# Kernel optimization log

Measured on AMD Instinct MI355X. Metric: run time of the kernel, lower is better.

Reference implementation:

```python
import jax, jax.numpy as jnp
import numpy as np

D_MODEL = 1024
NHEAD = 16
D_K = D_MODEL // NHEAD
NEG_INF = -1e30


def setup_inputs() -> dict:
    key = jax.random.key(0)
    ks = jax.random.split(key, 5)
    seq, batch = 2048, 4
    scale_in = 1.0 / np.sqrt(D_MODEL)
    return {
        "x": jax.random.normal(ks[0], (seq, batch, D_MODEL), dtype=jnp.float32),
        # torch nn.Linear stores weight as (out_features, in_features)
        "w_qkv": jax.random.normal(ks[1], (3 * D_MODEL, D_MODEL), dtype=jnp.float32) * scale_in,
        "b_qkv": jax.random.normal(ks[2], (3 * D_MODEL,), dtype=jnp.float32) * 0.01,
        "w_out": jax.random.normal(ks[3], (D_MODEL, D_MODEL), dtype=jnp.float32) * scale_in,
        "b_out": jax.random.normal(ks[4], (D_MODEL,), dtype=jnp.float32) * 0.01,
        "causal": 1,
    }


def reference(x, w_qkv, b_qkv, w_out, b_out, causal):
    seq, batch, d_model = x.shape
    # fused QKV projection: (seq, batch, 3*d_model)
    qkv = jnp.einsum("sbd,ed->sbe", x, w_qkv) + b_qkv
    q, k, v = jnp.split(qkv, 3, axis=-1)

    def to_heads(t):
        # (seq, batch, d_model) -> (batch*nhead, seq, d_k)
        return t.reshape(seq, batch * NHEAD, D_K).transpose(1, 0, 2)

    q, k, v = to_heads(q), to_heads(k), to_heads(v)
    # full O(seq^2) score tensor, matching the manual implementation
    scores = jnp.einsum("hqd,hkd->hqk", q, k) / (D_K ** 0.5)
    if causal:  # causal is a static Python int, safe under jit as constant
        mask = jnp.triu(jnp.ones((seq, seq), dtype=bool), k=1)
        scores = jnp.where(mask[None, :, :], NEG_INF, scores)
    attn = jax.nn.softmax(scores, axis=-1)
    out = jnp.einsum("hqk,hkd->hqd", attn, v)  # (batch*nhead, seq, d_k)
    out = out.transpose(1, 0, 2).reshape(seq, batch, d_model)
    return jnp.einsum("sbd,ed->sbe", out, w_out) + b_out
```

## Files before the change

### kernel.cpp

```cpp
#include <hip/hip_runtime.h>

typedef __attribute__((ext_vector_type(8))) short short8;
typedef __attribute__((ext_vector_type(4))) float floatx4;
typedef __attribute__((ext_vector_type(4))) unsigned short ushort4v;

__device__ __forceinline__ unsigned short f2bf(float f) {
  unsigned int u = __float_as_uint(f);
  u += 0x7FFFu + ((u >> 16) & 1u);
  return (unsigned short)(u >> 16);
}

__device__ __forceinline__ unsigned int cvt_pk_bf16(float lo, float hi) {
  unsigned int r;
  asm("v_cvt_pk_bf16_f32 %0, %1, %2" : "=v"(r) : "v"(lo), "v"(hi));
  return r;
}

__device__ __forceinline__ void async_copy16(const void* g, void* l) {
  __builtin_amdgcn_global_load_lds(
      (const __attribute__((address_space(1))) unsigned int*)g,
      (__attribute__((address_space(3))) unsigned int*)l, 16, 0, 0);
}

__device__ __forceinline__ float fexp2(float x) {
#if __has_builtin(__builtin_amdgcn_exp2f)
  return __builtin_amdgcn_exp2f(x);
#else
  return exp2f(x);
#endif
}

__global__ __launch_bounds__(256) void cvt_all(const float* __restrict__ x,
                                               const float* __restrict__ wq,
                                               const float* __restrict__ wo,
                                               unsigned short* __restrict__ Xb,
                                               unsigned short* __restrict__ Wqb,
                                               unsigned short* __restrict__ Wob) {
  int i = blockIdx.x * blockDim.x + threadIdx.x;
  const float* src;
  unsigned short* dst;
  int off;
  if (i < 2097152) { src = x;  dst = Xb;  off = i; }
  else if (i < 2883584) { src = wq; dst = Wqb; off = i - 2097152; }
  else { src = wo; dst = Wob; off = i - 2883584; }
  float4 v = reinterpret_cast<const float4*>(src)[off];
  ushort4v o;
  o[0] = f2bf(v.x); o[1] = f2bf(v.y); o[2] = f2bf(v.z); o[3] = f2bf(v.w);
  reinterpret_cast<ushort4v*>(dst)[off] = o;
}

template <int MODE, int NX>
__global__ __launch_bounds__(256, 4) void gemm_nt(const unsigned short* __restrict__ A,
                                                  const unsigned short* __restrict__ B,
                                                  const float* __restrict__ bias,
                                                  void* __restrict__ C,
                                                  int M, int N, int K) {
  __shared__ __align__(16) unsigned short lds[2][128 * 64];
  unsigned short* lA = lds[0];
  unsigned short* lB = lds[1];
  unsigned short* lflat = &lds[0][0];
  const int tid = threadIdx.x;
  const int lane = tid & 63, wave = tid >> 6;
  const int lr = lane & 15, lh = lane >> 4;
  const int chunk = gridDim.x >> 3;
  const int g2 = (blockIdx.x & 7) * chunk + (blockIdx.x >> 3);
  const int m0 = (g2 / NX) * 128, n0 = (g2 % NX) * 128;
  const int wm = (wave >> 1) * 64, wn = (wave & 1) * 64;
  floatx4 acc[4][4] = {};

  for (int k0 = 0; k0 < K; k0 += 64) {
    __syncthreads();
#pragma unroll
    for (int c0 = 0; c0 < 1024; c0 += 256) {
      int L = c0 + tid;
      int r = L >> 3;
      int c = (L & 7) ^ (r & 7);
      async_copy16(A + (size_t)(m0 + r) * K + k0 + c * 8, &lA[(size_t)(c0 + wave * 64) * 8]);
      async_copy16(B + (size_t)(n0 + r) * K + k0 + c * 8, &lB[(size_t)(c0 + wave * 64) * 8]);
    }
    __syncthreads();
#pragma unroll
    for (int kk = 0; kk < 2; ++kk) {
      short8 af[4], bfr[4];
#pragma unroll
      for (int mf = 0; mf < 4; ++mf)
        af[mf] = *(const short8*)&lA[(wm + mf * 16 + lr) * 64 + (((kk * 4 + lh) ^ (lr & 7)) * 8)];
#pragma unroll
      for (int nf = 0; nf < 4; ++nf)
        bfr[nf] = *(const short8*)&lB[(wn + nf * 16 + lr) * 64 + (((kk * 4 + lh) ^ (lr & 7)) * 8)];
#pragma unroll
      for (int mf = 0; mf < 4; ++mf)
#pragma unroll
        for (int nf = 0; nf < 4; ++nf)
          acc[mf][nf] = __builtin_amdgcn_mfma_f32_16x16x32_bf16(af[mf], bfr[nf], acc[mf][nf], 0, 0, 0);
    }
  }

  if (MODE == 1 && (n0 >> 10) == 2) {
    __syncthreads();
#pragma unroll
    for (int mf = 0; mf < 4; ++mf) {
      int sl = (wm >> 2) + mf * 4 + lh;
#pragma unroll
      for (int nf = 0; nf < 4; ++nf) {
        int cl = wn + nf * 16 + lr;
        int hh = cl >> 6, dd = cl & 63;
        int sx = sl ^ ((dd & 3) << 3);
#pragma unroll
        for (int r = 0; r < 4; ++r) {
          float v = acc[mf][nf][r] + bias[n0 + cl];
          lflat[((r * 2 + hh) * 64 + dd) * 32 + sx] = f2bf(v);
        }
      }
    }
    __syncthreads();
    const int hbase = (n0 & 1023) >> 6;
    const int s0g = m0 >> 2;
    unsigned short* V = (unsigned short*)C + (size_t)2 * 64 * 2048 * 64;
#pragma unroll
    for (int k = 0; k < 8; ++k) {
      int f = tid + k * 256;
      int p = f >> 2, q = f & 3;
      int b = p >> 7, hh = (p >> 6) & 1, dd = p & 63;
      int g = b * 16 + hbase + hh;
      int sc = (q ^ (dd & 3)) * 8;
      short8 vv = *(const short8*)&lflat[p * 32 + q * 8];
      *(short8*)&V[((size_t)g * 64 + dd) * 2048 + s0g + sc] = vv;
    }
  } else {
#pragma unroll
    for (int mf = 0; mf < 4; ++mf)
#pragma unroll
      for (int nf = 0; nf < 4; ++nf)
#pragma unroll
        for (int r = 0; r < 4; ++r) {
          int row = m0 + wm + mf * 16 + lh * 4 + r;
          int col = n0 + wn + nf * 16 + lr;
          float v = acc[mf][nf][r] + bias[col];
          if (MODE == 0) {
            ((float*)C)[(size_t)row * N + col] = v;
          } else {
            int part = col >> 10, wi = col & 1023;
            int h = wi >> 6, dd = wi & 63;
            int s = row >> 2, b = row & 3;
            int gg = b * 16 + h;
            size_t base = (size_t)part * (64u * 2048u * 64u);
            if (part == 0) v *= 0.18033688011112042f;
            ((unsigned short*)C)[base + ((size_t)gg * 2048 + s) * 64 + dd] = f2bf(v);
          }
        }
  }
}

__global__ __launch_bounds__(256, 3) void attn_fwd(const unsigned short* __restrict__ Qb,
                                                   const unsigned short* __restrict__ Kb,
                                                   const unsigned short* __restrict__ Vt,
                                                   unsigned short* __restrict__ Att,
                                                   const int* __restrict__ causal_p) {
  __shared__ __align__(16) unsigned short lK[2][64 * 64];
  __shared__ __align__(16) unsigned short lV[2][64 * 64];
  __shared__ __align__(16) unsigned short lP[4][32 * 64];
  const int tid = threadIdx.x;
  const int lane = tid & 63, w = tid >> 6;
  const int lr = lane & 15, lh = lane >> 4;
  const int bid = blockIdx.x;
  const int g = (bid & 7) + 8 * (bid >> 7);
  int qt = (bid >> 3) & 15;
  qt = (qt & 12) | ((qt ^ (qt >> 2)) & 3);
  const int q0 = qt * 128;
  const int causal = causal_p[0];
  const size_t headOff = (size_t)g * 2048 * 64;
  const size_t vtHead = (size_t)g * 64 * 2048;
  const int q0w = q0 + w * 32;

  short8 qf[2][2];
#pragma unroll
  for (int qb = 0; qb < 2; ++qb)
#pragma unroll
    for (int kf = 0; kf < 2; ++kf)
      qf[qb][kf] = *(const short8*)&Qb[headOff + (size_t)(q0w + qb * 16 + lr) * 64 + kf * 32 + lh * 8];

  floatx4 oacc[2][4] = {};
  float mrow[2] = {-1e30f, -1e30f}, lrow[2] = {0.f, 0.f};

  const int nt = causal ? (q0 + 128) / 64 : 2048 / 64;
  const int qmax_w = q0w + 31;

  auto stageK = [&](int buf, int kv0) {
#pragma unroll
    for (int c0 = 0; c0 < 512; c0 += 256) {
      int L = c0 + tid;
      int kvr = L >> 3;
      int c = (tid & 7) ^ (kvr & 7);
      async_copy16(Kb + headOff + (size_t)(kv0 + kvr) * 64 + c * 8,
                   &lK[buf][(size_t)(c0 + w * 64) * 8]);
    }
  };
  auto stageV = [&](int buf, int kv0) {
#pragma unroll
    for (int c0 = 0; c0 < 512; c0 += 256) {
      int L = c0 + tid;
      int dr = L >> 3;
      int c = (tid & 7) ^ (dr & 7);
      async_copy16(Vt + vtHead + (size_t)dr * 2048 + kv0 + c * 8,
                   &lV[buf][(size_t)(c0 + w * 64) * 8]);
    }
  };

  stageK(0, 0);
  stageV(0, 0);
  int cur = 0;

  for (int t = 0; t < nt; ++t) {
    const int kv0 = t * 64;
    if (t + 1 < nt) {
      stageK(cur ^ 1, kv0 + 64);
      stageV(cur ^ 1, kv0 + 64);
      asm volatile("s_waitcnt vmcnt(4)" ::: "memory");
    } else {
      asm volatile("s_waitcnt vmcnt(0)" ::: "memory");
    }
    __builtin_amdgcn_s_barrier();
    asm volatile("" ::: "memory");

    if (!causal || kv0 <= qmax_w) {
      floatx4 sacc[2][4] = {};
      __builtin_amdgcn_s_setprio(1);
#pragma unroll
      for (int kk = 0; kk < 2; ++kk) {
        short8 kfr[4];
#pragma unroll
        for (int nf = 0; nf < 4; ++nf)
          kfr[nf] = *(const short8*)&lK[cur][(nf * 16 + lr) * 64 + (((kk * 4 + lh) ^ (lr & 7)) * 8)];
#pragma unroll
        for (int qb = 0; qb < 2; ++qb)
#pragma unroll
          for (int nf = 0; nf < 4; ++nf)
            sacc[qb][nf] = __builtin_amdgcn_mfma_f32_16x16x32_bf16(kfr[nf], qf[qb][kk], sacc[qb][nf], 0, 0, 0);
      }
      __builtin_amdgcn_s_setprio(0);

      if (causal && kv0 + 63 > q0w) {
#pragma unroll
        for (int qb = 0; qb < 2; ++qb) {
          int q = q0w + qb * 16 + lr;
#pragma unroll
          for (int nf = 0; nf < 4; ++nf)
#pragma unroll
            for (int r = 0; r < 4; ++r) {
              int kv = kv0 + nf * 16 + lh * 4 + r;
              if (kv > q) sacc[qb][nf][r] = -1e30f;
            }
        }
      }

      float alpha[2];
#pragma unroll
      for (int qb = 0; qb < 2; ++qb) {
        float rm = -1e30f;
#pragma unroll
        for (int nf = 0; nf < 4; ++nf)
          rm = fmaxf(rm, fmaxf(fmaxf(sacc[qb][nf][0], sacc[qb][nf][1]),
                               fmaxf(sacc[qb][nf][2], sacc[qb][nf][3])));
        rm = fmaxf(rm, __shfl_xor(rm, 16, 64));
        rm = fmaxf(rm, __shfl_xor(rm, 32, 64));
        float mn = fmaxf(mrow[qb], rm);
        alpha[qb] = fexp2(mrow[qb] - mn);
        mrow[qb] = mn;
        float rs = 0.f;
#pragma unroll
        for (int nf = 0; nf < 4; ++nf)
#pragma unroll
          for (int r = 0; r < 4; ++r) {
            float p = fexp2(sacc[qb][nf][r] - mn);
            sacc[qb][nf][r] = p;
            rs += p;
          }
        rs += __shfl_xor(rs, 16, 64);
        rs += __shfl_xor(rs, 32, 64);
        lrow[qb] = lrow[qb] * alpha[qb] + rs;
      }

#pragma unroll
      for (int qb = 0; qb < 2; ++qb)
#pragma unroll
        for (int nf = 0; nf < 4; ++nf) {
          uint2 pk;
          pk.x = cvt_pk_bf16(sacc[qb][nf][0], sacc[qb][nf][1]);
          pk.y = cvt_pk_bf16(sacc[qb][nf][2], sacc[qb][nf][3]);
          int c = (2 * nf + (lh >> 1)) ^ (lr & 7);
          *(uint2*)&lP[w][(qb * 16 + lr) * 64 + c * 8 + (lh & 1) * 4] = pk;
        }

#pragma unroll
      for (int qb = 0; qb < 2; ++qb) {
        float at[4];
#pragma unroll
        for (int r = 0; r < 4; ++r)
          at[r] = __shfl(alpha[qb], lh * 4 + r, 64);
#pragma unroll
        for (int nd = 0; nd < 4; ++nd)
#pragma unroll
          for (int r = 0; r < 4; ++r)
            oacc[qb][nd][r] *= at[r];
      }

      __builtin_amdgcn_s_setprio(1);
#pragma unroll
      for (int kk = 0; kk < 2; ++kk) {
        short8 pf[2], vf[4];
#pragma unroll
        for (int qb = 0; qb < 2; ++qb)
          pf[qb] = *(const short8*)&lP[w][(qb * 16 + lr) * 64 + (((kk * 4 + lh) ^ (lr & 7)) * 8)];
#pragma unroll
        for (int nd = 0; nd < 4; ++nd)
          vf[nd] = *(const short8*)&lV[cur][(nd * 16 + lr) * 64 + (((kk * 4 + lh) ^ (lr & 7)) * 8)];
#pragma unroll
        for (int qb = 0; qb < 2; ++qb)
#pragma unroll
          for (int nd = 0; nd < 4; ++nd)
            oacc[qb][nd] = __builtin_amdgcn_mfma_f32_16x16x32_bf16(pf[qb], vf[nd], oacc[qb][nd], 0, 0, 0);
      }
      __builtin_amdgcn_s_setprio(0);
    }
    asm volatile("" ::: "memory");
    __builtin_amdgcn_s_barrier();
    cur ^= 1;
  }

  const int bb = g >> 4, hh = g & 15;
#pragma unroll
  for (int qb = 0; qb < 2; ++qb) {
    float invl = 1.f / lrow[qb];
    float it[4];
#pragma unroll
    for (int r = 0; r < 4; ++r)
      it[r] = __shfl(invl, lh * 4 + r, 64);
#pragma unroll
    for (int r = 0; r < 4; ++r) {
      int s = q0w + qb * 16 + lh * 4 + r;
#pragma unroll
      for (int nd = 0; nd < 4; ++nd) {
        int dd = nd * 16 + lr;
        Att[((size_t)s * 4 + bb) * 1024 + hh * 64 + dd] = f2bf(oacc[qb][nd][r] * it[r]);
      }
    }
  }
}

extern "C" void kernel_launch(void* const* d_in, const int* in_sizes, int n_in,
                              void* d_out, int out_size, void* d_ws, size_t ws_size,
                              hipStream_t stream) {
  const float* x     = (const float*)d_in[0];
  const float* w_qkv = (const float*)d_in[1];
  const float* b_qkv = (const float*)d_in[2];
  const float* w_out = (const float*)d_in[3];
  const float* b_out = (const float*)d_in[4];
  const int*   causal = (const int*)d_in[5];
  float* out = (float*)d_out;

  char* ws = (char*)d_ws;
  size_t off = 0;
  auto alloc = [&](size_t bytes) { char* p = ws + off; off += (bytes + 255) & ~(size_t)255; return p; };
  unsigned short* Xbf  = (unsigned short*)alloc((size_t)8192 * 1024 * 2);
  unsigned short* Wqkv = (unsigned short*)alloc((size_t)3072 * 1024 * 2);
  unsigned short* Wout = (unsigned short*)alloc((size_t)1024 * 1024 * 2);
  unsigned short* QKV  = (unsigned short*)alloc((size_t)3 * 64 * 2048 * 64 * 2);
  unsigned short* Att  = (unsigned short*)alloc((size_t)8192 * 1024 * 2);
  (void)ws_size; (void)in_sizes; (void)n_in; (void)out_size;

  cvt_all<<<12288, 256, 0, stream>>>(x, w_qkv, w_out, Xbf, Wqkv, Wout);

  gemm_nt<1, 24><<<24 * 64, 256, 0, stream>>>(Xbf, Wqkv, b_qkv, (void*)QKV, 8192, 3072, 1024);

  const unsigned short* Qh = QKV;
  const unsigned short* Kh = QKV + (size_t)64 * 2048 * 64;
  const unsigned short* Vh = QKV + (size_t)2 * 64 * 2048 * 64;
  attn_fwd<<<1024, 256, 0, stream>>>(Qh, Kh, Vh, Att, causal);

  gemm_nt<0, 8><<<8 * 64, 256, 0, stream>>>(Att, Wout, b_out, (void*)out, 8192, 1024, 1024);
}
```

Baseline: 176.2 us.

## Switch attention to 32x32x16 MFMA with register-resident P and staged output

Rewrites the attention inner loop to use 32x32x16 bf16 MFMA tiles, so each lane owns one query row. Row max and sum then need only one cross-lane shuffle, and the alpha broadcast shuffles go away. P is moved into the B-operand layout with lane-swap shuffles instead of a round trip through LDS, which removes the per-wave P buffer. The output is staged through shared memory so the global stores are 16-byte rows instead of scattered 2-byte writes. The launch-bounds occupancy hint is dropped, so register pressure and occupancy may change.

After: 176.7 us. About the same (+0.3%).

```diff
diff --git a/kernel.cpp b/kernel.cpp
--- a/kernel.cpp
+++ b/kernel.cpp
@@ -2,6 +2,7 @@
 
 typedef __attribute__((ext_vector_type(8))) short short8;
 typedef __attribute__((ext_vector_type(4))) float floatx4;
+typedef __attribute__((ext_vector_type(16))) float floatx16;
 typedef __attribute__((ext_vector_type(4))) unsigned short ushort4v;
 
 __device__ __forceinline__ unsigned short f2bf(float f) {
@@ -152,17 +153,15 @@
   }
 }
 
-__global__ __launch_bounds__(256, 3) void attn_fwd(const unsigned short* __restrict__ Qb,
-                                                   const unsigned short* __restrict__ Kb,
-                                                   const unsigned short* __restrict__ Vt,
-                                                   unsigned short* __restrict__ Att,
-                                                   const int* __restrict__ causal_p) {
-  __shared__ __align__(16) unsigned short lK[2][64 * 64];
-  __shared__ __align__(16) unsigned short lV[2][64 * 64];
-  __shared__ __align__(16) unsigned short lP[4][32 * 64];
+__global__ __launch_bounds__(256) void attn_fwd(const unsigned short* __restrict__ Qb,
+                                                const unsigned short* __restrict__ Kb,
+                                                const unsigned short* __restrict__ Vt,
+                                                unsigned short* __restrict__ Att,
+                                                const int* __restrict__ causal_p) {
+  __shared__ __align__(16) unsigned short smem[16384];
   const int tid = threadIdx.x;
   const int lane = tid & 63, w = tid >> 6;
-  const int lr = lane & 15, lh = lane >> 4;
+  const int l31 = lane & 31, hi = lane >> 5;
   const int bid = blockIdx.x;
   const int g = (bid & 7) + 8 * (bid >> 7);
   int qt = (bid >> 3) & 15;
@@ -172,16 +171,15 @@
   const size_t headOff = (size_t)g * 2048 * 64;
   const size_t vtHead = (size_t)g * 64 * 2048;
   const int q0w = q0 + w * 32;
-
-  short8 qf[2][2];
-#pragma unroll
-  for (int qb = 0; qb < 2; ++qb)
-#pragma unroll
-    for (int kf = 0; kf < 2; ++kf)
-      qf[qb][kf] = *(const short8*)&Qb[headOff + (size_t)(q0w + qb * 16 + lr) * 64 + kf * 32 + lh * 8];
-
-  floatx4 oacc[2][4] = {};
-  float mrow[2] = {-1e30f, -1e30f}, lrow[2] = {0.f, 0.f};
+  const int qg = q0w + l31;
+
+  short8 qf[4];
+#pragma unroll
+  for (int c = 0; c < 4; ++c)
+    qf[c] = *(const short8*)&Qb[headOff + (size_t)qg * 64 + c * 16 + hi * 8];
+
+  floatx16 oacc[2] = {};
+  float mrow = -1e30f, lrow = 0.f;
 
   const int nt = causal ? (q0 + 128) / 64 : 2048 / 64;
   const int qmax_w = q0w + 31;
@@ -193,7 +191,7 @@
       int kvr = L >> 3;
       int c = (tid & 7) ^ (kvr & 7);
       async_copy16(Kb + headOff + (size_t)(kv0 + kvr) * 64 + c * 8,
-                   &lK[buf][(size_t)(c0 + w * 64) * 8]);
+                   &smem[(size_t)buf * 4096 + (size_t)(c0 + w * 64) * 8]);
     }
   };
   auto stageV = [&](int buf, int kv0) {
@@ -203,7 +201,7 @@
       int dr = L >> 3;
       int c = (tid & 7) ^ (dr & 7);
       async_copy16(Vt + vtHead + (size_t)dr * 2048 + kv0 + c * 8,
-                   &lV[buf][(size_t)(c0 + w * 64) * 8]);
+                   &smem[8192 + (size_t)buf * 4096 + (size_t)(c0 + w * 64) * 8]);
     }
   };
 
@@ -224,127 +222,114 @@
     asm volatile("" ::: "memory");
 
     if (!causal || kv0 <= qmax_w) {
-      floatx4 sacc[2][4] = {};
+      const unsigned short* lK = &smem[(size_t)cur * 4096];
+      const unsigned short* lV = &smem[8192 + (size_t)cur * 4096];
+
+      floatx16 sacc[2] = {};
       __builtin_amdgcn_s_setprio(1);
 #pragma unroll
-      for (int kk = 0; kk < 2; ++kk) {
-        short8 kfr[4];
-#pragma unroll
-        for (int nf = 0; nf < 4; ++nf)
-          kfr[nf] = *(const short8*)&lK[cur][(nf * 16 + lr) * 64 + (((kk * 4 + lh) ^ (lr & 7)) * 8)];
-#pragma unroll
-        for (int qb = 0; qb < 2; ++qb)
-#pragma unroll
-          for (int nf = 0; nf < 4; ++nf)
-            sacc[qb][nf] = __builtin_amdgcn_mfma_f32_16x16x32_bf16(kfr[nf], qf[qb][kk], sacc[qb][nf], 0, 0, 0);
+      for (int st = 0; st < 2; ++st)
+#pragma unroll
+        for (int c = 0; c < 4; ++c) {
+          int row = st * 32 + l31;
+          short8 kf = *(const short8*)&lK[row * 64 + (((2 * c + hi) ^ (row & 7)) * 8)];
+          sacc[st] = __builtin_amdgcn_mfma_f32_32x32x16_bf16(kf, qf[c], sacc[st], 0, 0, 0);
+        }
+      __builtin_amdgcn_s_setprio(0);
+
+      if (causal && kv0 + 63 > q0w) {
+#pragma unroll
+        for (int st = 0; st < 2; ++st)
+#pragma unroll
+          for (int r = 0; r < 16; ++r) {
+            int kv = kv0 + st * 32 + (r & 3) + 8 * (r >> 2) + 4 * hi;
+            if (kv > qg) sacc[st][r] = -1e30f;
+          }
       }
-      __builtin_amdgcn_s_setprio(0);
-
-      if (causal && kv0 + 63 > q0w) {
-#pragma unroll
-        for (int qb = 0; qb < 2; ++qb) {
-          int q = q0w + qb * 16 + lr;
-#pragma unroll
-          for (int nf = 0; nf < 4; ++nf)
-#pragma unroll
-            for (int r = 0; r < 4; ++r) {
-              int kv = kv0 + nf * 16 + lh * 4 + r;
-              if (kv > q) sacc[qb][nf][r] = -1e30f;
-            }
-        }
-      }
-
-      float alpha[2];
-#pragma unroll
-      for (int qb = 0; qb < 2; ++qb) {
-        float rm = -1e30f;
-#pragma unroll
-        for (int nf = 0; nf < 4; ++nf)
-          rm = fmaxf(rm, fmaxf(fmaxf(sacc[qb][nf][0], sacc[qb][nf][1]),
-                               fmaxf(sacc[qb][nf][2], sacc[qb][nf][3])));
-        rm = fmaxf(rm, __shfl_xor(rm, 16, 64));
-        rm = fmaxf(rm, __shfl_xor(rm, 32, 64));
-        float mn = fmaxf(mrow[qb], rm);
-        alpha[qb] = fexp2(mrow[qb] - mn);
-        mrow[qb] = mn;
-        float rs = 0.f;
-#pragma unroll
-        for (int nf = 0; nf < 4; ++nf)
-#pragma unroll
-          for (int r = 0; r < 4; ++r) {
-            float p = fexp2(sacc[qb][nf][r] - mn);
-            sacc[qb][nf][r] = p;
-            rs += p;
+
+      float rm = -1e30f;
+#pragma unroll
+      for (int st = 0; st < 2; ++st)
+#pragma unroll
+        for (int r = 0; r < 16; ++r)
+          rm = fmaxf(rm, sacc[st][r]);
+      rm = fmaxf(rm, __shfl_xor(rm, 32, 64));
+      float mn = fmaxf(mrow, rm);
+      float alpha = fexp2(mrow - mn);
+      mrow = mn;
+      float rs = 0.f;
+#pragma unroll
+      for (int st = 0; st < 2; ++st)
+#pragma unroll
+        for (int r = 0; r < 16; ++r) {
+          float p = fexp2(sacc[st][r] - mn);
+          sacc[st][r] = p;
+          rs += p;
+        }
+      rs += __shfl_xor(rs, 32, 64);
+      lrow = lrow * alpha + rs;
+#pragma unroll
+      for (int dt = 0; dt < 2; ++dt)
+#pragma unroll
+        for (int r = 0; r < 16; ++r)
+          oacc[dt][r] *= alpha;
+
+#pragma unroll
+      for (int st = 0; st < 2; ++st)
+#pragma unroll
+        for (int h = 0; h < 2; ++h) {
+          unsigned int C1 = cvt_pk_bf16(sacc[st][8 * h + 0], sacc[st][8 * h + 1]);
+          unsigned int C2 = cvt_pk_bf16(sacc[st][8 * h + 2], sacc[st][8 * h + 3]);
+          unsigned int C3 = cvt_pk_bf16(sacc[st][8 * h + 4], sacc[st][8 * h + 5]);
+          unsigned int C4 = cvt_pk_bf16(sacc[st][8 * h + 6], sacc[st][8 * h + 7]);
+          unsigned int P1 = hi ? C1 : C3, P2 = hi ? C2 : C4;
+          unsigned int R1 = (unsigned int)__shfl_xor((int)P1, 32, 64);
+          unsigned int R2 = (unsigned int)__shfl_xor((int)P2, 32, 64);
+          union { unsigned int u[4]; short8 s; } pf;
+          pf.u[0] = hi ? R1 : C1; pf.u[1] = hi ? R2 : C2;
+          pf.u[2] = hi ? C3 : R1; pf.u[3] = hi ? C4 : R2;
+          __builtin_amdgcn_s_setprio(1);
+#pragma unroll
+          for (int dt = 0; dt < 2; ++dt) {
+            int row = dt * 32 + l31;
+            short8 vf = *(const short8*)&lV[row * 64 + (((st * 4 + h * 2 + hi) ^ (row & 7)) * 8)];
+            oacc[dt] = __builtin_amdgcn_mfma_f32_32x32x16_bf16(vf, pf.s, oacc[dt], 0, 0, 0);
           }
-        rs += __shfl_xor(rs, 16, 64);
-        rs += __shfl_xor(rs, 32, 64);
-        lrow[qb] = lrow[qb] * alpha[qb] + rs;
-      }
-
-#pragma unroll
-      for (int qb = 0; qb < 2; ++qb)
-#pragma unroll
-        for (int nf = 0; nf < 4; ++nf) {
-          uint2 pk;
-          pk.x = cvt_pk_bf16(sacc[qb][nf][0], sacc[qb][nf][1]);
-          pk.y = cvt_pk_bf16(sacc[qb][nf][2], sacc[qb][nf][3]);
-          int c = (2 * nf + (lh >> 1)) ^ (lr & 7);
-          *(uint2*)&lP[w][(qb * 16 + lr) * 64 + c * 8 + (lh & 1) * 4] = pk;
-        }
-
-#pragma unroll
-      for (int qb = 0; qb < 2; ++qb) {
-        float at[4];
-#pragma unroll
-        for (int r = 0; r < 4; ++r)
-          at[r] = __shfl(alpha[qb], lh * 4 + r, 64);
-#pragma unroll
-        for (int nd = 0; nd < 4; ++nd)
-#pragma unroll
-          for (int r = 0; r < 4; ++r)
-            oacc[qb][nd][r] *= at[r];
-      }
-
-      __builtin_amdgcn_s_setprio(1);
-#pragma unroll
-      for (int kk = 0; kk < 2; ++kk) {
-        short8 pf[2], vf[4];
-#pragma unroll
-        for (int qb = 0; qb < 2; ++qb)
-          pf[qb] = *(const short8*)&lP[w][(qb * 16 + lr) * 64 + (((kk * 4 + lh) ^ (lr & 7)) * 8)];
-#pragma unroll
-        for (int nd = 0; nd < 4; ++nd)
-          vf[nd] = *(const short8*)&lV[cur][(nd * 16 + lr) * 64 + (((kk * 4 + lh) ^ (lr & 7)) * 8)];
-#pragma unroll
-        for (int qb = 0; qb < 2; ++qb)
-#pragma unroll
-          for (int nd = 0; nd < 4; ++nd)
-            oacc[qb][nd] = __builtin_amdgcn_mfma_f32_16x16x32_bf16(pf[qb], vf[nd], oacc[qb][nd], 0, 0, 0);
-      }
-      __builtin_amdgcn_s_setprio(0);
+          __builtin_amdgcn_s_setprio(0);
+        }
     }
     asm volatile("" ::: "memory");
     __builtin_amdgcn_s_barrier();
     cur ^= 1;
   }
 
+  float inv = 1.f / lrow;
+#pragma unroll
+  for (int dt = 0; dt < 2; ++dt)
+#pragma unroll
+    for (int r = 0; r < 16; ++r)
+      oacc[dt][r] *= inv;
+
+  unsigned short* ov = smem;
+  const int ql = w * 32 + l31;
+#pragma unroll
+  for (int dt = 0; dt < 2; ++dt)
+#pragma unroll
+    for (int tt = 0; tt < 4; ++tt) {
+      int d0 = dt * 32 + 8 * tt + 4 * hi;
+      uint2 pk;
+      pk.x = cvt_pk_bf16(oacc[dt][4 * tt + 0], oacc[dt][4 * tt + 1]);
+      pk.y = cvt_pk_bf16(oacc[dt][4 * tt + 2], oacc[dt][4 * tt + 3]);
+      *(uint2*)&ov[ql * 68 + d0] = pk;
+    }
+  __syncthreads();
   const int bb = g >> 4, hh = g & 15;
 #pragma unroll
-  for (int qb = 0; qb < 2; ++qb) {
-    float invl = 1.f / lrow[qb];
-    float it[4];
-#pragma unroll
-    for (int r = 0; r < 4; ++r)
-      it[r] = __shfl(invl, lh * 4 + r, 64);
-#pragma unroll
-    for (int r = 0; r < 4; ++r) {
-      int s = q0w + qb * 16 + lh * 4 + r;
-#pragma unroll
-      for (int nd = 0; nd < 4; ++nd) {
-        int dd = nd * 16 + lr;
-        Att[((size_t)s * 4 + bb) * 1024 + hh * 64 + dd] = f2bf(oacc[qb][nd][r] * it[r]);
-      }
-    }
+  for (int k = 0; k < 4; ++k) {
+    int row = (tid >> 3) + k * 32;
+    short8 vv = *(const short8*)&ov[row * 68 + (tid & 7) * 8];
+    int sg = q0 + row;
+    *(short8*)&Att[((size_t)sg * 4 + bb) * 1024 + hh * 64 + (tid & 7) * 8] = vv;
   }
 }
 
```
